# Kernel optimization log

Measured on AMD Instinct MI355X. Metric: run time of the kernel, lower is better.

Reference implementation:

```python
import jax, jax.numpy as jnp
import numpy as np

N_NODES = 50000
N_EDGES = 800000
N_GRAPHS = 256
NEG_SLOPE = 0.2  # PyG GATConv default leaky_relu slope


def gat_conv(x, edge_index, W, a_src, a_dst, bias, concat):
    # x: [N, F_in], edge_index: [2, E] (row=source, col=dest), W: [F_in, H*C]
    N = x.shape[0]
    H, C = a_src.shape
    h = (x @ W).reshape(N, H, C)                       # [N, H, C]
    s_src = (h * a_src).sum(-1)                        # [N, H]
    s_dst = (h * a_dst).sum(-1)                        # [N, H]
    src, dst = edge_index[0], edge_index[1]
    alpha = jax.nn.leaky_relu(s_src[src] + s_dst[dst], NEG_SLOPE)  # [E, H]
    # softmax over edges grouped by destination node
    m = jax.ops.segment_max(alpha, dst, num_segments=N)
    alpha = jnp.exp(alpha - m[dst])
    denom = jax.ops.segment_sum(alpha, dst, num_segments=N)
    alpha = alpha / (denom[dst] + 1e-16)
    out = jax.ops.segment_sum(h[src] * alpha[:, :, None], dst, num_segments=N)  # [N, H, C]
    out = out.reshape(N, H * C) if concat else out.mean(axis=1)
    return out + bias


def setup_inputs() -> dict:
    key = jax.random.key(0)
    ks = jax.random.split(key, 12)
    x = jax.random.normal(ks[0], (N_NODES, 27), dtype=jnp.float32)
    edge_index = jax.random.randint(ks[1], (2, N_EDGES), 0, N_NODES, dtype=jnp.int64 if jax.config.jax_enable_x64 else jnp.int32)
    batch = (jnp.arange(N_NODES) * N_GRAPHS) // N_NODES  # sorted, every graph non-empty
    g = lambda k, shape, fan_in: jax.random.normal(k, shape, dtype=jnp.float32) * (1.0 / np.sqrt(fan_in))
    return {
        "x": x, "edge_index": edge_index, "batch": batch,
        "W1": g(ks[2], (27, 64), 27), "a_src1": g(ks[3], (4, 16), 16), "a_dst1": g(ks[4], (4, 16), 16), "b1": jnp.zeros((64,), jnp.float32),
        "W2": g(ks[5], (64, 256), 64), "a_src2": g(ks[6], (1, 256), 256), "a_dst2": g(ks[7], (1, 256), 256), "b2": jnp.zeros((256,), jnp.float32),
        "Wl1": g(ks[8], (256, 512), 256), "bl1": jnp.zeros((512,), jnp.float32),
        "Wl2": g(ks[9], (512, 1024), 512), "bl2": jnp.zeros((1024,), jnp.float32),
        "Wl3": g(ks[10], (1024, 4), 1024), "bl3": jnp.zeros((4,), jnp.float32),
    }


def reference(x, edge_index, batch, W1, a_src1, a_dst1, b1, W2, a_src2, a_dst2, b2, Wl1, bl1, Wl2, bl2, Wl3, bl3):
    N = x.shape[0]
    # add self loops (PyG GATConv default)
    loops = jnp.arange(N, dtype=edge_index.dtype)
    ei = jnp.concatenate([edge_index, jnp.stack([loops, loops])], axis=1)
    h = jax.nn.elu(gat_conv(x, ei, W1, a_src1, a_dst1, b1, concat=True))    # [N, 64]
    h = jax.nn.elu(gat_conv(h, ei, W2, a_src2, a_dst2, b2, concat=False))   # [N, 256]
    # global max pool per graph
    pooled = jax.ops.segment_max(h, batch, num_segments=N_GRAPHS)           # [G, 256]
    z = jax.nn.relu(pooled @ Wl1 + bl1)
    z = jax.nn.relu(z @ Wl2 + bl2)
    return z @ Wl3 + bl3                                                    # [G, 4] logits (CrossEntropyLoss branch)
```

## Files before the change

### kernel.cpp

```cpp
#include <hip/hip_runtime.h>
#include <hip/hip_fp16.h>
#include <math.h>

#define NEG_SLOPE 0.2f
#define SCANB 256
#define CAP 6144

__device__ __forceinline__ float leaky(float x) { return x >= 0.f ? x : NEG_SLOPE * x; }
__device__ __forceinline__ float elu(float x) { return x > 0.f ? x : expm1f(x); }

typedef _Float16 half8 __attribute__((ext_vector_type(8)));
typedef float floatx4 __attribute__((ext_vector_type(4)));


__global__ __launch_bounds__(1024) void k_passA(const int* __restrict__ src,
                                                const int* __restrict__ dst, int E, int nbuck,
                                                int2* __restrict__ tmp, int* __restrict__ bcursor) {
    __shared__ int cnt[256];
    __shared__ int base[256];
    int t = threadIdx.x;
    if (t < 256) cnt[t] = 0;
    __syncthreads();
    int e0 = blockIdx.x * 4096;
    int s[4], d[4], r[4];
    bool v[4];
#pragma unroll
    for (int i = 0; i < 4; ++i) {
        int e = e0 + i * 1024 + t;
        v[i] = e < E;
        if (v[i]) {
            s[i] = src[e];
            d[i] = dst[e];
            r[i] = atomicAdd(&cnt[d[i] >> 8], 1);
        }
    }
    __syncthreads();
    if (t < nbuck) {
        int c = cnt[t];
        base[t] = c ? atomicAdd(&bcursor[t], c) : 0;
    }
    __syncthreads();
#pragma unroll
    for (int i = 0; i < 4; ++i) {
        if (v[i]) {
            int b = d[i] >> 8;
            int pos = base[b] + r[i];
            if (pos < CAP) tmp[(size_t)b * CAP + pos] = make_int2(s[i], d[i]);
        }
    }
}

__global__ __launch_bounds__(256) void k_B1(const int2* __restrict__ tmp,
                                            const int* __restrict__ bcursor,
                                            int* __restrict__ deg, int N) {
    __shared__ int cnt[256];
    int b = blockIdx.x, t = threadIdx.x;
    cnt[t] = 0;
    __syncthreads();
    int n = bcursor[b];
    if (n > CAP) n = CAP;
    for (int j = t; j < n; j += 256) {
        int d = tmp[(size_t)b * CAP + j].y;
        atomicAdd(&cnt[d & 255], 1);
    }
    __syncthreads();
    int node = b * 256 + t;
    if (node < N) deg[node] = cnt[t] + 1;
}

__global__ void k_scan1(const int* __restrict__ in, int* __restrict__ out,
                        int* __restrict__ bsum, int N) {
    __shared__ int sm[SCANB];
    int i = blockIdx.x * SCANB + threadIdx.x;
    int v = (i < N) ? in[i] : 0;
    sm[threadIdx.x] = v;
    __syncthreads();
    for (int off = 1; off < SCANB; off <<= 1) {
        int t = (threadIdx.x >= off) ? sm[threadIdx.x - off] : 0;
        __syncthreads();
        sm[threadIdx.x] += t;
        __syncthreads();
    }
    if (i < N) out[i] = sm[threadIdx.x] - v;
    if (threadIdx.x == SCANB - 1) bsum[blockIdx.x] = sm[SCANB - 1];
}

__global__ void k_scan2(int* __restrict__ bsum, int nb) {
    __shared__ int sm[SCANB];
    int v = (threadIdx.x < nb) ? bsum[threadIdx.x] : 0;
    sm[threadIdx.x] = v;
    __syncthreads();
    for (int off = 1; off < SCANB; off <<= 1) {
        int t = (threadIdx.x >= off) ? sm[threadIdx.x - off] : 0;
        __syncthreads();
        sm[threadIdx.x] += t;
        __syncthreads();
    }
    if (threadIdx.x < nb) bsum[threadIdx.x] = sm[threadIdx.x] - v;
}

__global__ void k_scan3(int* __restrict__ out, const int* __restrict__ bsum,
                        int* __restrict__ csr, int N) {
    int i = blockIdx.x * SCANB + threadIdx.x;
    if (i < N) {
        int v = out[i] + bsum[blockIdx.x];
        out[i] = v;
        csr[v] = i;
    }
}

__global__ __launch_bounds__(256) void k_B2(const int2* __restrict__ tmp,
                                            const int* __restrict__ bcursor,
                                            const int* __restrict__ offs,
                                            int* __restrict__ csr, int N) {
    __shared__ int cnt[256];
    int b = blockIdx.x, t = threadIdx.x;
    cnt[t] = 0;
    __syncthreads();
    int n = bcursor[b];
    if (n > CAP) n = CAP;
    for (int j = t; j < n; j += 256) {
        int2 sd = tmp[(size_t)b * CAP + j];
        int r = atomicAdd(&cnt[sd.y & 255], 1);
        csr[offs[sd.y] + 1 + r] = sd.x;
    }
}

__global__ void k_prep(const float* __restrict__ W2, __half* __restrict__ W2t,
                       const float* __restrict__ Wl1, __half* __restrict__ Wl1t,
                       const float* __restrict__ Wl2, __half* __restrict__ Wl2t,
                       const float* __restrict__ a_src2, const float* __restrict__ a_dst2,
                       float* __restrict__ ws2, float* __restrict__ wd2) {
    int i = blockIdx.x * blockDim.x + threadIdx.x;
    if (i < 16384) {
        int k = i >> 8, n = i & 255;
        W2t[(size_t)n * 64 + k] = __float2half(W2[i]);
    } else if (i < 16384 + 131072) {
        int j = i - 16384;
        int k = j >> 9, n = j & 511;
        Wl1t[(size_t)n * 256 + k] = __float2half(Wl1[j]);
    } else if (i < 16384 + 131072 + 524288) {
        int j = i - 16384 - 131072;
        int k = j >> 10, n = j & 1023;
        Wl2t[(size_t)n * 512 + k] = __float2half(Wl2[j]);
    } else if (i < 16384 + 131072 + 524288 + 128) {
        int j = i - 16384 - 131072 - 524288;
        int k = j & 63;
        const float* av = (j < 64) ? a_src2 : a_dst2;
        float acc = 0.f;
        for (int c = 0; c < 256; ++c) acc += W2[k * 256 + c] * av[c];
        if (j < 64) ws2[k] = acc; else wd2[k] = acc;
    }
}


__global__ void k_h1(const float* __restrict__ x, const float* __restrict__ W1,
                     const float* __restrict__ a_src, const float* __restrict__ a_dst,
                     __half* __restrict__ h1h, float* __restrict__ ssrc, float* __restrict__ sdst,
                     int N) {
    __shared__ float sW[27 * 64];
    for (int i = threadIdx.x; i < 27 * 64; i += blockDim.x) sW[i] = W1[i];
    __syncthreads();
    int wave = threadIdx.x >> 6;
    int lane = threadIdx.x & 63;
    int n = blockIdx.x * 4 + wave;
    if (n >= N) return;
    const float* xr = x + (size_t)n * 27;
    float acc = 0.f;
#pragma unroll
    for (int k = 0; k < 27; ++k) acc += xr[k] * sW[k * 64 + lane];
    h1h[(size_t)n * 64 + lane] = __float2half(acc);
    int hd = lane >> 4, c = lane & 15;
    float vs = acc * a_src[hd * 16 + c];
    float vd = acc * a_dst[hd * 16 + c];
#pragma unroll
    for (int off = 8; off >= 1; off >>= 1) {
        vs += __shfl_xor(vs, off);
        vd += __shfl_xor(vd, off);
    }
    if (c == 0) {
        ssrc[n * 4 + hd] = vs;
        sdst[n * 4 + hd] = vd;
    }
}

__global__ void k_msd1(const int* __restrict__ csr, const int* __restrict__ offs,
                       const int* __restrict__ deg,
                       const float* __restrict__ ssrc, const float* __restrict__ sdst,
                       __half* __restrict__ e4h, float* __restrict__ dinv4, int N) {
    int i = blockIdx.x * blockDim.x + threadIdx.x;
    if (i >= N * 4) return;
    int n = i >> 2, hd = i & 3;
    int start = offs[n], dg = deg[n];
    float sd = sdst[(size_t)n * 4 + hd];
    float m = -INFINITY;
    for (int j = 0; j < dg; ++j) {
        int s = csr[start + j];
        m = fmaxf(m, leaky(ssrc[(size_t)s * 4 + hd] + sd));
    }
    float den = 0.f;
    for (int j = 0; j < dg; ++j) {
        int s = csr[start + j];
        float e = expf(leaky(ssrc[(size_t)s * 4 + hd] + sd) - m);
        den += e;
        e4h[(size_t)(start + j) * 4 + hd] = __float2half(e);
    }
    dinv4[(size_t)n * 4 + hd] = 1.f / (den + 1e-16f);
}

__global__ __launch_bounds__(64) void k_agg1(
        const int* __restrict__ csr, const int* __restrict__ offs, const int* __restrict__ deg,
        const __half* __restrict__ e4h, const float* __restrict__ dinv4,
        const __half* __restrict__ h1h, const float* __restrict__ bias,
        const float* __restrict__ ws2, const float* __restrict__ wd2,
        __half* __restrict__ out, float* __restrict__ ssrc2, float* __restrict__ sdst2, int N) {
    int d = blockIdx.x;
    int lane = threadIdx.x;
    int start = offs[d], dg = deg[d];
    int hd = lane >> 4;
    float acc = 0.f;
#pragma unroll 4
    for (int j = 0; j < dg; ++j) {
        int s = csr[start + j];
        float w = __half2float(e4h[(size_t)(start + j) * 4 + hd]);
        acc += __half2float(h1h[(size_t)s * 64 + lane]) * w;
    }
    acc *= dinv4[(size_t)d * 4 + hd];
    float av = elu(acc + bias[lane]);
    out[(size_t)d * 64 + lane] = __float2half(av);
    float vs = av * ws2[lane];
    float vd = av * wd2[lane];
#pragma unroll
    for (int off = 32; off >= 1; off >>= 1) {
        vs += __shfl_xor(vs, off);
        vd += __shfl_xor(vd, off);
    }
    if (lane == 0) { ssrc2[d] = vs; sdst2[d] = vd; }
}


__global__ void k_msd2(const int* __restrict__ csr, const int* __restrict__ offs,
                       const int* __restrict__ deg,
                       const float* __restrict__ ssrc, const float* __restrict__ sdst,
                       __half* __restrict__ e1h, float* __restrict__ dinv1, int N) {
    int n = blockIdx.x * blockDim.x + threadIdx.x;
    if (n >= N) return;
    int start = offs[n], dg = deg[n];
    float sd = sdst[n];
    float m = -INFINITY;
    for (int j = 0; j < dg; ++j) {
        int s = csr[start + j];
        m = fmaxf(m, leaky(ssrc[s] + sd));
    }
    float den = 0.f;
    for (int j = 0; j < dg; ++j) {
        int s = csr[start + j];
        float e = expf(leaky(ssrc[s] + sd) - m);
        den += e;
        e1h[start + j] = __float2half(e);
    }
    dinv1[n] = 1.f / (den + 1e-16f);
}

__global__ __launch_bounds__(64) void k_agg2(
        const int* __restrict__ csr, const int* __restrict__ offs, const int* __restrict__ deg,
        const __half* __restrict__ e1h, const float* __restrict__ dinv1,
        const __half* __restrict__ act1h, __half* __restrict__ aggh, int N) {
    int d = blockIdx.x;
    int lane = threadIdx.x;
    int start = offs[d], dg = deg[d];
    float acc = 0.f;
#pragma unroll 4
    for (int j = 0; j < dg; ++j) {
        int s = csr[start + j];
        float w = __half2float(e1h[start + j]);
        acc += __half2float(act1h[(size_t)s * 64 + lane]) * w;
    }
    acc *= dinv1[d];
    aggh[(size_t)d * 64 + lane] = __float2half(acc);
}

__global__ void k_h2b(const __half* __restrict__ aggh, const __half* __restrict__ W2t,
                      const float* __restrict__ b2, __half* __restrict__ act2h, int N) {
    int t = threadIdx.x;
    int wv = t >> 6, lane = t & 63;
    int lr = lane & 15, lg = lane >> 4;
    int n0 = blockIdx.x * 16;

    half8 a0 = {0, 0, 0, 0, 0, 0, 0, 0};
    half8 a1 = {0, 0, 0, 0, 0, 0, 0, 0};
    int nodeA = n0 + lr;
    if (nodeA < N) {
        a0 = *(const half8*)(aggh + (size_t)nodeA * 64 + lg * 8);
        a1 = *(const half8*)(aggh + (size_t)nodeA * 64 + 32 + lg * 8);
    }
#pragma unroll
    for (int c = 0; c < 4; ++c) {
        int col = wv * 64 + c * 16 + lr;
        half8 b0 = *(const half8*)(W2t + (size_t)col * 64 + lg * 8);
        half8 b1 = *(const half8*)(W2t + (size_t)col * 64 + 32 + lg * 8);
        floatx4 acc = {0.f, 0.f, 0.f, 0.f};
        acc = __builtin_amdgcn_mfma_f32_16x16x32_f16(a0, b0, acc, 0, 0, 0);
        acc = __builtin_amdgcn_mfma_f32_16x16x32_f16(a1, b1, acc, 0, 0, 0);
        float bv = b2[col];
#pragma unroll
        for (int r = 0; r < 4; ++r) {
            int node = n0 + lg * 4 + r;
            if (node < N) act2h[(size_t)node * 256 + col] = __float2half(elu(acc[r] + bv));
        }
    }
}


__global__ void k_pool(const __half* __restrict__ act2h, const int* __restrict__ batch, int N,
                       __half* __restrict__ pooledh) {
    int g = blockIdx.x;
    int t = threadIdx.x;
    int lo = 0, hi = N;
    while (lo < hi) { int mid = (lo + hi) >> 1; if (batch[mid] < g) lo = mid + 1; else hi = mid; }
    int start = lo;
    lo = start; hi = N;
    while (lo < hi) { int mid = (lo + hi) >> 1; if (batch[mid] < g + 1) lo = mid + 1; else hi = mid; }
    int end = lo;
    float m = -INFINITY;
    for (int n = start; n < end; ++n) m = fmaxf(m, __half2float(act2h[(size_t)n * 256 + t]));
    pooledh[g * 256 + t] = __float2half(m);
}

__global__ void k_gemm(const __half* __restrict__ A, const __half* __restrict__ Wt,
                       const float* __restrict__ bias, __half* __restrict__ C,
                       int M, int N, int K, int relu) {
    int t = threadIdx.x;
    int wv = t >> 6, lane = t & 63;
    int lr = lane & 15, lg = lane >> 4;
    int bx = blockIdx.x, by = blockIdx.y;
    int arow = by * 64 + wv * 16 + lr;
    floatx4 acc[4] = {{0.f,0.f,0.f,0.f},{0.f,0.f,0.f,0.f},{0.f,0.f,0.f,0.f},{0.f,0.f,0.f,0.f}};
    for (int k0 = 0; k0 < K; k0 += 32) {
        half8 a = *(const half8*)(A + (size_t)arow * K + k0 + lg * 8);
#pragma unroll
        for (int c = 0; c < 4; ++c) {
            int col = bx * 64 + c * 16 + lr;
            half8 b = *(const half8*)(Wt + (size_t)col * K + k0 + lg * 8);
            acc[c] = __builtin_amdgcn_mfma_f32_16x16x32_f16(a, b, acc[c], 0, 0, 0);
        }
    }
#pragma unroll
    for (int c = 0; c < 4; ++c) {
        int col = bx * 64 + c * 16 + lr;
        float bv = bias[col];
#pragma unroll
        for (int r = 0; r < 4; ++r) {
            int row = by * 64 + wv * 16 + lg * 4 + r;
            float v = acc[c][r] + bv;
            if (relu) v = fmaxf(v, 0.f);
            C[(size_t)row * N + col] = __float2half(v);
        }
    }
}

__global__ void k_mlp3(const __half* __restrict__ z2, const float* __restrict__ Wl3,
                       const float* __restrict__ bl3, float* __restrict__ out, int G) {
    __shared__ float sT[16];
    int g = blockIdx.x, t = threadIdx.x;
    int wave = t >> 6, lane = t & 63;
    float p[4] = {0.f, 0.f, 0.f, 0.f};
#pragma unroll
    for (int kk = 0; kk < 4; ++kk) {
        int k = t + kk * 256;
        float z = __half2float(z2[(size_t)g * 1024 + k]);
        float4 w = ((const float4*)Wl3)[k];
        p[0] += z * w.x; p[1] += z * w.y; p[2] += z * w.z; p[3] += z * w.w;
    }
#pragma unroll
    for (int c = 0; c < 4; ++c) {
#pragma unroll
        for (int off = 32; off >= 1; off >>= 1) p[c] += __shfl_xor(p[c], off);
        if (lane == 0) sT[wave * 4 + c] = p[c];
    }
    __syncthreads();
    if (t < 4) {
        float v = bl3[t] + sT[t] + sT[4 + t] + sT[8 + t] + sT[12 + t];
        out[(size_t)g * 4 + t] = v;
    }
}

extern "C" void kernel_launch(void* const* d_in, const int* in_sizes, int n_in,
                              void* d_out, int out_size, void* d_ws, size_t ws_size,
                              hipStream_t stream) {
    const float* x      = (const float*)d_in[0];
    const int*   ei     = (const int*)d_in[1];
    const int*   batch  = (const int*)d_in[2];
    const float* W1     = (const float*)d_in[3];
    const float* a_src1 = (const float*)d_in[4];
    const float* a_dst1 = (const float*)d_in[5];
    const float* b1     = (const float*)d_in[6];
    const float* W2     = (const float*)d_in[7];
    const float* a_src2 = (const float*)d_in[8];
    const float* a_dst2 = (const float*)d_in[9];
    const float* b2     = (const float*)d_in[10];
    const float* Wl1    = (const float*)d_in[11];
    const float* bl1    = (const float*)d_in[12];
    const float* Wl2    = (const float*)d_in[13];
    const float* bl2    = (const float*)d_in[14];
    const float* Wl3    = (const float*)d_in[15];
    const float* bl3    = (const float*)d_in[16];

    const int N = in_sizes[0] / 27;
    const int E = in_sizes[1] / 2;
    const int G = out_size / 4;
    const int EN = E + N;
    const int nbuck = (N + 255) >> 8;

    const int* srcA = ei;
    const int* dstA = ei + E;

    char* wp = (char*)d_ws;
    int2* tmp    = (int2*)wp; wp += (size_t)256 * CAP * 8;
    int* bcursor = (int*)wp; wp += 256 * 4;
    int* deg     = (int*)wp; wp += (size_t)N * 4;
    int* offs    = (int*)wp; wp += (size_t)N * 4;
    int* bsum    = (int*)wp; wp += (size_t)SCANB * 4;
    int* csr     = (int*)wp; wp += (size_t)EN * 4;

    float* ssrc1 = (float*)wp; wp += (size_t)N * 4 * 4;
    float* sdst1 = (float*)wp; wp += (size_t)N * 4 * 4;
    float* ssrc2 = (float*)wp; wp += (size_t)N * 4;
    float* sdst2 = (float*)wp; wp += (size_t)N * 4;
    float* dinv4 = (float*)wp; wp += (size_t)N * 4 * 4;
    float* dinv1 = (float*)wp; wp += (size_t)N * 4;
    float* ws2   = (float*)wp; wp += 64 * 4;
    float* wd2   = (float*)wp; wp += 64 * 4;

    __half* h1h   = (__half*)wp; wp += (size_t)N * 64 * 2;
    __half* act1h = (__half*)wp; wp += (size_t)N * 64 * 2;
    __half* aggh  = (__half*)wp; wp += (size_t)N * 64 * 2;
    __half* act2h = (__half*)wp; wp += (size_t)N * 256 * 2;
    __half* e4h   = (__half*)wp; wp += (size_t)EN * 4 * 2;
    __half* e1h   = (__half*)wp; wp += (size_t)EN * 2;
    __half* W2t   = (__half*)wp; wp += (size_t)64 * 256 * 2;
    __half* Wl1t  = (__half*)wp; wp += (size_t)512 * 256 * 2;
    __half* Wl2t  = (__half*)wp; wp += (size_t)1024 * 512 * 2;
    __half* pooledh = (__half*)wp; wp += (size_t)G * 256 * 2;
    __half* z1h   = (__half*)wp; wp += (size_t)G * 512 * 2;
    __half* z2h   = (__half*)wp; wp += (size_t)G * 1024 * 2;

    const int nb = (N + SCANB - 1) / SCANB;

    {
        int tot = 16384 + 131072 + 524288 + 128;
        k_prep<<<(tot + 255) / 256, 256, 0, stream>>>(W2, W2t, Wl1, Wl1t, Wl2, Wl2t,
                                                      a_src2, a_dst2, ws2, wd2);
    }

    hipMemsetAsync(bcursor, 0, 256 * 4, stream);
    k_passA<<<(E + 4095) / 4096, 1024, 0, stream>>>(srcA, dstA, E, nbuck, tmp, bcursor);
    k_B1<<<nbuck, 256, 0, stream>>>(tmp, bcursor, deg, N);
    k_scan1<<<nb, SCANB, 0, stream>>>(deg, offs, bsum, N);
    k_scan2<<<1, SCANB, 0, stream>>>(bsum, nb);
    k_scan3<<<nb, SCANB, 0, stream>>>(offs, bsum, csr, N);
    k_B2<<<nbuck, 256, 0, stream>>>(tmp, bcursor, offs, csr, N);

    k_h1<<<(N + 3) / 4, 256, 0, stream>>>(x, W1, a_src1, a_dst1, h1h, ssrc1, sdst1, N);
    k_msd1<<<(N * 4 + 255) / 256, 256, 0, stream>>>(csr, offs, deg, ssrc1, sdst1, e4h, dinv4, N);
    k_agg1<<<N, 64, 0, stream>>>(csr, offs, deg, e4h, dinv4, h1h, b1, ws2, wd2,
                                 act1h, ssrc2, sdst2, N);

    k_msd2<<<(N + 255) / 256, 256, 0, stream>>>(csr, offs, deg, ssrc2, sdst2, e1h, dinv1, N);
    k_agg2<<<N, 64, 0, stream>>>(csr, offs, deg, e1h, dinv1, act1h, aggh, N);
    k_h2b<<<(N + 15) / 16, 256, 0, stream>>>(aggh, W2t, b2, act2h, N);

    k_pool<<<G, 256, 0, stream>>>(act2h, batch, N, pooledh);
    k_gemm<<<dim3(512 / 64, 256 / 64), 256, 0, stream>>>(pooledh, Wl1t, bl1, z1h, 256, 512, 256, 1);
    k_gemm<<<dim3(1024 / 64, 256 / 64), 256, 0, stream>>>(z1h, Wl2t, bl2, z2h, 256, 1024, 512, 1);
    k_mlp3<<<G, 256, 0, stream>>>(z2h, Wl3, bl3, (float*)d_out, G);
}
```

Before: 258.1 us.

## Fuse degree count with block scan, vectorize softmax and split-edge aggregation

Merges the degree-count kernel with the per-block scan and drops the separate deg array in favour of offs[n+1]-offs[n]. The layer-1 softmax now handles one node per thread across all four heads, using float4 gathers and packed half4 weight stores. Both aggregation kernels now have each half-wavefront process alternate edges with half2 loads, then combine the halves with a cross-lane shuffle. These changes aim to cut index and weight loads, kernel launches and gather latency, at the cost of extra shuffles and lower thread-level parallelism in msd1.

```diff
diff --git a/kernel.cpp b/kernel.cpp
--- a/kernel.cpp
+++ b/kernel.cpp
@@ -8,6 +8,8 @@
 
 __device__ __forceinline__ float leaky(float x) { return x >= 0.f ? x : NEG_SLOPE * x; }
 __device__ __forceinline__ float elu(float x) { return x > 0.f ? x : expm1f(x); }
+
+struct Half4 { __half2 a, b; };
 
 typedef _Float16 half8 __attribute__((ext_vector_type(8)));
 typedef float floatx4 __attribute__((ext_vector_type(4)));
@@ -50,29 +52,37 @@
     }
 }
 
-__global__ __launch_bounds__(256) void k_B1(const int2* __restrict__ tmp,
-                                            const int* __restrict__ bcursor,
-                                            int* __restrict__ deg, int N) {
+__global__ __launch_bounds__(256) void k_B1s(const int2* __restrict__ tmp,
+                                             const int* __restrict__ bcursor,
+                                             int* __restrict__ offs, int* __restrict__ bsum,
+                                             int N) {
     __shared__ int cnt[256];
+    __shared__ int sm[256];
     int b = blockIdx.x, t = threadIdx.x;
     cnt[t] = 0;
     __syncthreads();
     int n = bcursor[b];
     if (n > CAP) n = CAP;
-    for (int j = t; j < n; j += 256) {
-        int d = tmp[(size_t)b * CAP + j].y;
-        atomicAdd(&cnt[d & 255], 1);
-    }
+    for (int j = t; j < n; j += 256)
+        atomicAdd(&cnt[tmp[(size_t)b * CAP + j].y & 255], 1);
     __syncthreads();
     int node = b * 256 + t;
-    if (node < N) deg[node] = cnt[t] + 1;
-}
-
-__global__ void k_scan1(const int* __restrict__ in, int* __restrict__ out,
-                        int* __restrict__ bsum, int N) {
+    int v = (node < N) ? cnt[t] + 1 : 0;
+    sm[t] = v;
+    __syncthreads();
+    for (int off = 1; off < 256; off <<= 1) {
+        int u = (t >= off) ? sm[t - off] : 0;
+        __syncthreads();
+        sm[t] += u;
+        __syncthreads();
+    }
+    if (node < N) offs[node] = sm[t] - v;
+    if (t == 255) bsum[b] = sm[255];
+}
+
+__global__ void k_scan2(int* __restrict__ bsum, int nb) {
     __shared__ int sm[SCANB];
-    int i = blockIdx.x * SCANB + threadIdx.x;
-    int v = (i < N) ? in[i] : 0;
+    int v = (threadIdx.x < nb) ? bsum[threadIdx.x] : 0;
     sm[threadIdx.x] = v;
     __syncthreads();
     for (int off = 1; off < SCANB; off <<= 1) {
@@ -81,31 +91,17 @@
         sm[threadIdx.x] += t;
         __syncthreads();
     }
-    if (i < N) out[i] = sm[threadIdx.x] - v;
-    if (threadIdx.x == SCANB - 1) bsum[blockIdx.x] = sm[SCANB - 1];
-}
-
-__global__ void k_scan2(int* __restrict__ bsum, int nb) {
-    __shared__ int sm[SCANB];
-    int v = (threadIdx.x < nb) ? bsum[threadIdx.x] : 0;
-    sm[threadIdx.x] = v;
-    __syncthreads();
-    for (int off = 1; off < SCANB; off <<= 1) {
-        int t = (threadIdx.x >= off) ? sm[threadIdx.x - off] : 0;
-        __syncthreads();
-        sm[threadIdx.x] += t;
-        __syncthreads();
-    }
     if (threadIdx.x < nb) bsum[threadIdx.x] = sm[threadIdx.x] - v;
 }
 
-__global__ void k_scan3(int* __restrict__ out, const int* __restrict__ bsum,
-                        int* __restrict__ csr, int N) {
+__global__ void k_scan3(int* __restrict__ offs, const int* __restrict__ bsum,
+                        int* __restrict__ csr, int N, int EN) {
     int i = blockIdx.x * SCANB + threadIdx.x;
     if (i < N) {
-        int v = out[i] + bsum[blockIdx.x];
-        out[i] = v;
+        int v = offs[i] + bsum[blockIdx.x];
+        offs[i] = v;
         csr[v] = i;
+        if (i == N - 1) offs[N] = EN;
     }
 }
 
@@ -185,53 +181,108 @@
 }
 
 __global__ void k_msd1(const int* __restrict__ csr, const int* __restrict__ offs,
-                       const int* __restrict__ deg,
                        const float* __restrict__ ssrc, const float* __restrict__ sdst,
-                       __half* __restrict__ e4h, float* __restrict__ dinv4, int N) {
-    int i = blockIdx.x * blockDim.x + threadIdx.x;
-    if (i >= N * 4) return;
-    int n = i >> 2, hd = i & 3;
-    int start = offs[n], dg = deg[n];
-    float sd = sdst[(size_t)n * 4 + hd];
-    float m = -INFINITY;
-    for (int j = 0; j < dg; ++j) {
+                       Half4* __restrict__ e4h, float* __restrict__ dinv4, int N) {
+    int n = blockIdx.x * blockDim.x + threadIdx.x;
+    if (n >= N) return;
+    int start = offs[n];
+    int dg = offs[n + 1] - start;
+    float4 sd = ((const float4*)sdst)[n];
+    float m0 = -INFINITY, m1 = -INFINITY, m2 = -INFINITY, m3 = -INFINITY;
+    int j = 0;
+    for (; j + 4 <= dg; j += 4) {
+        int s0 = csr[start + j], s1 = csr[start + j + 1];
+        int s2 = csr[start + j + 2], s3 = csr[start + j + 3];
+        float4 a0 = ((const float4*)ssrc)[s0];
+        float4 a1 = ((const float4*)ssrc)[s1];
+        float4 a2 = ((const float4*)ssrc)[s2];
+        float4 a3 = ((const float4*)ssrc)[s3];
+        m0 = fmaxf(fmaxf(m0, leaky(a0.x + sd.x)),
+                   fmaxf(leaky(a1.x + sd.x), fmaxf(leaky(a2.x + sd.x), leaky(a3.x + sd.x))));
+        m1 = fmaxf(fmaxf(m1, leaky(a0.y + sd.y)),
+                   fmaxf(leaky(a1.y + sd.y), fmaxf(leaky(a2.y + sd.y), leaky(a3.y + sd.y))));
+        m2 = fmaxf(fmaxf(m2, leaky(a0.z + sd.z)),
+                   fmaxf(leaky(a1.z + sd.z), fmaxf(leaky(a2.z + sd.z), leaky(a3.z + sd.z))));
+        m3 = fmaxf(fmaxf(m3, leaky(a0.w + sd.w)),
+                   fmaxf(leaky(a1.w + sd.w), fmaxf(leaky(a2.w + sd.w), leaky(a3.w + sd.w))));
+    }
+    for (; j < dg; ++j) {
         int s = csr[start + j];
-        m = fmaxf(m, leaky(ssrc[(size_t)s * 4 + hd] + sd));
-    }
-    float den = 0.f;
-    for (int j = 0; j < dg; ++j) {
+        float4 a = ((const float4*)ssrc)[s];
+        m0 = fmaxf(m0, leaky(a.x + sd.x));
+        m1 = fmaxf(m1, leaky(a.y + sd.y));
+        m2 = fmaxf(m2, leaky(a.z + sd.z));
+        m3 = fmaxf(m3, leaky(a.w + sd.w));
+    }
+    float d0 = 0.f, d1 = 0.f, d2 = 0.f, d3 = 0.f;
+#pragma unroll 2
+    for (j = 0; j < dg; ++j) {
         int s = csr[start + j];
-        float e = expf(leaky(ssrc[(size_t)s * 4 + hd] + sd) - m);
-        den += e;
-        e4h[(size_t)(start + j) * 4 + hd] = __float2half(e);
-    }
-    dinv4[(size_t)n * 4 + hd] = 1.f / (den + 1e-16f);
+        float4 a = ((const float4*)ssrc)[s];
+        float e0 = expf(leaky(a.x + sd.x) - m0);
+        float e1 = expf(leaky(a.y + sd.y) - m1);
+        float e2 = expf(leaky(a.z + sd.z) - m2);
+        float e3 = expf(leaky(a.w + sd.w) - m3);
+        d0 += e0; d1 += e1; d2 += e2; d3 += e3;
+        Half4 h;
+        h.a = __floats2half2_rn(e0, e1);
+        h.b = __floats2half2_rn(e2, e3);
+        e4h[start + j] = h;
+    }
+    float4 di;
+    di.x = 1.f / (d0 + 1e-16f);
+    di.y = 1.f / (d1 + 1e-16f);
+    di.z = 1.f / (d2 + 1e-16f);
+    di.w = 1.f / (d3 + 1e-16f);
+    ((float4*)dinv4)[n] = di;
 }
 
 __global__ __launch_bounds__(64) void k_agg1(
-        const int* __restrict__ csr, const int* __restrict__ offs, const int* __restrict__ deg,
-        const __half* __restrict__ e4h, const float* __restrict__ dinv4,
+        const int* __restrict__ csr, const int* __restrict__ offs,
+        const Half4* __restrict__ e4h, const float* __restrict__ dinv4,
         const __half* __restrict__ h1h, const float* __restrict__ bias,
         const float* __restrict__ ws2, const float* __restrict__ wd2,
         __half* __restrict__ out, float* __restrict__ ssrc2, float* __restrict__ sdst2, int N) {
     int d = blockIdx.x;
     int lane = threadIdx.x;
-    int start = offs[d], dg = deg[d];
-    int hd = lane >> 4;
-    float acc = 0.f;
+    int c = lane & 31, half = lane >> 5;
+    int hd = c >> 3;
+    int start = offs[d];
+    int dg = offs[d + 1] - start;
+    const __half* e4p = (const __half*)e4h;
+    float ax = 0.f, ay = 0.f;
 #pragma unroll 4
-    for (int j = 0; j < dg; ++j) {
-        int s = csr[start + j];
-        float w = __half2float(e4h[(size_t)(start + j) * 4 + hd]);
-        acc += __half2float(h1h[(size_t)s * 64 + lane]) * w;
-    }
-    acc *= dinv4[(size_t)d * 4 + hd];
-    float av = elu(acc + bias[lane]);
-    out[(size_t)d * 64 + lane] = __float2half(av);
-    float vs = av * ws2[lane];
-    float vd = av * wd2[lane];
-#pragma unroll
-    for (int off = 32; off >= 1; off >>= 1) {
+    for (int j0 = 0; j0 < dg; j0 += 2) {
+        int j = j0 + half;
+        int s = d;
+        float w = 0.f;
+        if (j < dg) {
+            s = csr[start + j];
+            w = __half2float(e4p[(size_t)(start + j) * 4 + hd]);
+        }
+        __half2 hv = *(const __half2*)(h1h + (size_t)s * 64 + 2 * c);
+        float2 f = __half22float2(hv);
+        ax += f.x * w;
+        ay += f.y * w;
+    }
+    ax += __shfl_xor(ax, 32);
+    ay += __shfl_xor(ay, 32);
+    float vs = 0.f, vd = 0.f;
+    float av0 = 0.f, av1 = 0.f;
+    if (lane < 32) {
+        float di = dinv4[(size_t)d * 4 + hd];
+        float2 b = ((const float2*)bias)[c];
+        av0 = elu(ax * di + b.x);
+        av1 = elu(ay * di + b.y);
+        __half2 o = __floats2half2_rn(av0, av1);
+        *(__half2*)(out + (size_t)d * 64 + 2 * c) = o;
+        float2 w1 = ((const float2*)ws2)[c];
+        float2 w2 = ((const float2*)wd2)[c];
+        vs = av0 * w1.x + av1 * w1.y;
+        vd = av0 * w2.x + av1 * w2.y;
+    }
+#pragma unroll
+    for (int off = 16; off >= 1; off >>= 1) {
         vs += __shfl_xor(vs, off);
         vd += __shfl_xor(vd, off);
     }
@@ -240,22 +291,27 @@
 
 
 __global__ void k_msd2(const int* __restrict__ csr, const int* __restrict__ offs,
-                       const int* __restrict__ deg,
                        const float* __restrict__ ssrc, const float* __restrict__ sdst,
                        __half* __restrict__ e1h, float* __restrict__ dinv1, int N) {
     int n = blockIdx.x * blockDim.x + threadIdx.x;
     if (n >= N) return;
-    int start = offs[n], dg = deg[n];
+    int start = offs[n];
+    int dg = offs[n + 1] - start;
     float sd = sdst[n];
     float m = -INFINITY;
-    for (int j = 0; j < dg; ++j) {
-        int s = csr[start + j];
-        m = fmaxf(m, leaky(ssrc[s] + sd));
-    }
+    int j = 0;
+    for (; j + 4 <= dg; j += 4) {
+        int s0 = csr[start + j], s1 = csr[start + j + 1];
+        int s2 = csr[start + j + 2], s3 = csr[start + j + 3];
+        float a0 = ssrc[s0], a1 = ssrc[s1], a2 = ssrc[s2], a3 = ssrc[s3];
+        m = fmaxf(fmaxf(m, leaky(a0 + sd)),
+                  fmaxf(leaky(a1 + sd), fmaxf(leaky(a2 + sd), leaky(a3 + sd))));
+    }
+    for (; j < dg; ++j) m = fmaxf(m, leaky(ssrc[csr[start + j]] + sd));
     float den = 0.f;
-    for (int j = 0; j < dg; ++j) {
-        int s = csr[start + j];
-        float e = expf(leaky(ssrc[s] + sd) - m);
+#pragma unroll 2
+    for (j = 0; j < dg; ++j) {
+        float e = expf(leaky(ssrc[csr[start + j]] + sd) - m);
         den += e;
         e1h[start + j] = __float2half(e);
     }
@@ -263,21 +319,36 @@
 }
 
 __global__ __launch_bounds__(64) void k_agg2(
-        const int* __restrict__ csr, const int* __restrict__ offs, const int* __restrict__ deg,
+        const int* __restrict__ csr, const int* __restrict__ offs,
         const __half* __restrict__ e1h, const float* __restrict__ dinv1,
         const __half* __restrict__ act1h, __half* __restrict__ aggh, int N) {
     int d = blockIdx.x;
     int lane = threadIdx.x;
-    int start = offs[d], dg = deg[d];
-    float acc = 0.f;
+    int c = lane & 31, half = lane >> 5;
+    int start = offs[d];
+    int dg = offs[d + 1] - start;
+    float ax = 0.f, ay = 0.f;
 #pragma unroll 4
-    for (int j = 0; j < dg; ++j) {
-        int s = csr[start + j];
-        float w = __half2float(e1h[start + j]);
-        acc += __half2float(act1h[(size_t)s * 64 + lane]) * w;
-    }
-    acc *= dinv1[d];
-    aggh[(size_t)d * 64 + lane] = __float2half(acc);
+    for (int j0 = 0; j0 < dg; j0 += 2) {
+        int j = j0 + half;
+        int s = d;
+        float w = 0.f;
+        if (j < dg) {
+            s = csr[start + j];
+            w = __half2float(e1h[start + j]);
+        }
+        __half2 hv = *(const __half2*)(act1h + (size_t)s * 64 + 2 * c);
+        float2 f = __half22float2(hv);
+        ax += f.x * w;
+        ay += f.y * w;
+    }
+    ax += __shfl_xor(ax, 32);
+    ay += __shfl_xor(ay, 32);
+    if (lane < 32) {
+        float di = dinv1[d];
+        __half2 o = __floats2half2_rn(ax * di, ay * di);
+        *(__half2*)(aggh + (size_t)d * 64 + 2 * c) = o;
+    }
 }
 
 __global__ void k_h2b(const __half* __restrict__ aggh, const __half* __restrict__ W2t,
@@ -416,34 +487,35 @@
     const int* dstA = ei + E;
 
     char* wp = (char*)d_ws;
-    int2* tmp    = (int2*)wp; wp += (size_t)256 * CAP * 8;
-    int* bcursor = (int*)wp; wp += 256 * 4;
-    int* deg     = (int*)wp; wp += (size_t)N * 4;
-    int* offs    = (int*)wp; wp += (size_t)N * 4;
-    int* bsum    = (int*)wp; wp += (size_t)SCANB * 4;
-    int* csr     = (int*)wp; wp += (size_t)EN * 4;
-
-    float* ssrc1 = (float*)wp; wp += (size_t)N * 4 * 4;
-    float* sdst1 = (float*)wp; wp += (size_t)N * 4 * 4;
-    float* ssrc2 = (float*)wp; wp += (size_t)N * 4;
-    float* sdst2 = (float*)wp; wp += (size_t)N * 4;
-    float* dinv4 = (float*)wp; wp += (size_t)N * 4 * 4;
-    float* dinv1 = (float*)wp; wp += (size_t)N * 4;
-    float* ws2   = (float*)wp; wp += 64 * 4;
-    float* wd2   = (float*)wp; wp += 64 * 4;
-
-    __half* h1h   = (__half*)wp; wp += (size_t)N * 64 * 2;
-    __half* act1h = (__half*)wp; wp += (size_t)N * 64 * 2;
-    __half* aggh  = (__half*)wp; wp += (size_t)N * 64 * 2;
-    __half* act2h = (__half*)wp; wp += (size_t)N * 256 * 2;
-    __half* e4h   = (__half*)wp; wp += (size_t)EN * 4 * 2;
-    __half* e1h   = (__half*)wp; wp += (size_t)EN * 2;
-    __half* W2t   = (__half*)wp; wp += (size_t)64 * 256 * 2;
-    __half* Wl1t  = (__half*)wp; wp += (size_t)512 * 256 * 2;
-    __half* Wl2t  = (__half*)wp; wp += (size_t)1024 * 512 * 2;
-    __half* pooledh = (__half*)wp; wp += (size_t)G * 256 * 2;
-    __half* z1h   = (__half*)wp; wp += (size_t)G * 512 * 2;
-    __half* z2h   = (__half*)wp; wp += (size_t)G * 1024 * 2;
+    auto take = [&](size_t bytes) { char* p = wp; wp += (bytes + 15) & ~(size_t)15; return p; };
+
+    int2* tmp     = (int2*)take((size_t)256 * CAP * 8);
+    int* bcursor  = (int*)take(256 * 4);
+    int* offs     = (int*)take((size_t)(N + 1) * 4);
+    int* bsum     = (int*)take((size_t)SCANB * 4);
+    int* csr      = (int*)take((size_t)EN * 4);
+
+    float* ssrc1  = (float*)take((size_t)N * 4 * 4);
+    float* sdst1  = (float*)take((size_t)N * 4 * 4);
+    float* ssrc2  = (float*)take((size_t)N * 4);
+    float* sdst2  = (float*)take((size_t)N * 4);
+    float* dinv4  = (float*)take((size_t)N * 4 * 4);
+    float* dinv1  = (float*)take((size_t)N * 4);
+    float* ws2    = (float*)take(64 * 4);
+    float* wd2    = (float*)take(64 * 4);
+
+    __half* h1h   = (__half*)take((size_t)N * 64 * 2);
+    __half* act1h = (__half*)take((size_t)N * 64 * 2);
+    __half* aggh  = (__half*)take((size_t)N * 64 * 2);
+    __half* act2h = (__half*)take((size_t)N * 256 * 2);
+    Half4* e4h    = (Half4*)take((size_t)EN * 8);
+    __half* e1h   = (__half*)take((size_t)EN * 2);
+    __half* W2t   = (__half*)take((size_t)64 * 256 * 2);
+    __half* Wl1t  = (__half*)take((size_t)512 * 256 * 2);
+    __half* Wl2t  = (__half*)take((size_t)1024 * 512 * 2);
+    __half* pooledh = (__half*)take((size_t)G * 256 * 2);
+    __half* z1h   = (__half*)take((size_t)G * 512 * 2);
+    __half* z2h   = (__half*)take((size_t)G * 1024 * 2);
 
     const int nb = (N + SCANB - 1) / SCANB;
 
@@ -455,19 +527,18 @@
 
     hipMemsetAsync(bcursor, 0, 256 * 4, stream);
     k_passA<<<(E + 4095) / 4096, 1024, 0, stream>>>(srcA, dstA, E, nbuck, tmp, bcursor);
-    k_B1<<<nbuck, 256, 0, stream>>>(tmp, bcursor, deg, N);
-    k_scan1<<<nb, SCANB, 0, stream>>>(deg, offs, bsum, N);
+    k_B1s<<<nbuck, 256, 0, stream>>>(tmp, bcursor, offs, bsum, N);
     k_scan2<<<1, SCANB, 0, stream>>>(bsum, nb);
-    k_scan3<<<nb, SCANB, 0, stream>>>(offs, bsum, csr, N);
+    k_scan3<<<nb, SCANB, 0, stream>>>(offs, bsum, csr, N, EN);
     k_B2<<<nbuck, 256, 0, stream>>>(tmp, bcursor, offs, csr, N);
 
     k_h1<<<(N + 3) / 4, 256, 0, stream>>>(x, W1, a_src1, a_dst1, h1h, ssrc1, sdst1, N);
-    k_msd1<<<(N * 4 + 255) / 256, 256, 0, stream>>>(csr, offs, deg, ssrc1, sdst1, e4h, dinv4, N);
-    k_agg1<<<N, 64, 0, stream>>>(csr, offs, deg, e4h, dinv4, h1h, b1, ws2, wd2,
+    k_msd1<<<(N + 255) / 256, 256, 0, stream>>>(csr, offs, ssrc1, sdst1, e4h, dinv4, N);
+    k_agg1<<<N, 64, 0, stream>>>(csr, offs, e4h, dinv4, h1h, b1, ws2, wd2,
                                  act1h, ssrc2, sdst2, N);
 
-    k_msd2<<<(N + 255) / 256, 256, 0, stream>>>(csr, offs, deg, ssrc2, sdst2, e1h, dinv1, N);
-    k_agg2<<<N, 64, 0, stream>>>(csr, offs, deg, e1h, dinv1, act1h, aggh, N);
+    k_msd2<<<(N + 255) / 256, 256, 0, stream>>>(csr, offs, ssrc2, sdst2, e1h, dinv1, N);
+    k_agg2<<<N, 64, 0, stream>>>(csr, offs, e1h, dinv1, act1h, aggh, N);
     k_h2b<<<(N + 15) / 16, 256, 0, stream>>>(aggh, W2t, b2, act2h, N);
 
     k_pool<<<G, 256, 0, stream>>>(act2h, batch, N, pooledh);
```

After: 271.3 us. +5.1%, slower.
